# Kernel tuning notes

Hardware: AMD Instinct MI355X
Metric: run time of the kernel (lower is better)

Reference implementation:

```python
import jax, jax.numpy as jnp
import numpy as np

EMB = 128
HEADS = 4
OUT = EMB // HEADS
NL = 50000
NR = 50000
E = 800000


def setup_inputs() -> dict:
    key = jax.random.key(0)
    ks = jax.random.split(key, 20)
    s = 0.05  # param init scale
    f32 = jnp.float32
    return {
        "left_features": jax.random.normal(ks[0], (NL, EMB), f32),
        "edge_indices": jax.random.randint(ks[1], (2, E), 0, NL),  # NL == NR
        "edge_features": jax.random.normal(ks[2], (E, EMB), f32),
        "right_features": jax.random.normal(ks[3], (NR, EMB), f32),
        # GATv2Conv params
        "W_l": jax.random.normal(ks[4], (EMB, HEADS * OUT), f32) * s,
        "b_l": jnp.zeros((HEADS * OUT,), f32),
        "W_r": jax.random.normal(ks[5], (EMB, HEADS * OUT), f32) * s,
        "b_r": jnp.zeros((HEADS * OUT,), f32),
        "W_e": jax.random.normal(ks[6], (EMB, HEADS * OUT), f32) * s,
        "att": jax.random.normal(ks[7], (HEADS, OUT), f32) * s,
        "b_conv": jnp.zeros((HEADS * OUT,), f32),
        # LayerNorm
        "ln_g": jnp.ones((EMB,), f32),
        "ln_b": jnp.zeros((EMB,), f32),
        # output MLP
        "W1": jax.random.normal(ks[8], (2 * EMB, EMB), f32) * s,
        "b1": jnp.zeros((EMB,), f32),
        "W2": jax.random.normal(ks[9], (EMB, EMB), f32) * s,
        "b2": jnp.zeros((EMB,), f32),
    }


def reference(left_features, edge_indices, edge_features, right_features,
              W_l, b_l, W_r, b_r, W_e, att, b_conv, ln_g, ln_b,
              W1, b1, W2, b2):
    H, O = att.shape
    n_right = right_features.shape[0]
    src = edge_indices[0]
    dst = edge_indices[1]

    # linear projections (GATv2: separate lin_l for src, lin_r for dst, lin_edge no bias)
    x_l = (left_features @ W_l + b_l).reshape(-1, H, O)   # [NL,H,O]
    x_r = (right_features @ W_r + b_r).reshape(-1, H, O)  # [NR,H,O]
    e = (edge_features @ W_e).reshape(-1, H, O)           # [E,H,O]

    # per-edge GATv2 attention logits
    z = jax.nn.leaky_relu(x_l[src] + x_r[dst] + e, 0.2)   # [E,H,O]
    logits = jnp.einsum('eho,ho->eh', z, att)             # [E,H]

    # segment softmax over destination nodes
    m = jax.ops.segment_max(logits, dst, num_segments=n_right)
    m = jnp.where(jnp.isfinite(m), m, 0.0)  # guard empty segments
    ex = jnp.exp(logits - m[dst])
    den = jax.ops.segment_sum(ex, dst, num_segments=n_right)
    alpha = ex / (den[dst] + 1e-16)                       # [E,H]

    # message = transformed src feature weighted by alpha, scatter-add to dst
    msg = jax.ops.segment_sum(x_l[src] * alpha[:, :, None], dst,
                              num_segments=n_right)       # [NR,H,O]
    msg = msg.reshape(n_right, H * O) + b_conv            # concat heads + bias

    # LayerNorm
    mu = jnp.mean(msg, axis=-1, keepdims=True)
    var = jnp.mean(jnp.square(msg - mu), axis=-1, keepdims=True)
    msg = (msg - mu) * jax.lax.rsqrt(var + 1e-5) * ln_g + ln_b

    # out MLP on [msg, right_features]
    h = jnp.concatenate([msg, right_features], axis=-1)
    h = jax.nn.relu(h @ W1 + b1)
    return h @ W2 + b2
```

## Files before the change

### kernel.cpp

```cpp
#include <hip/hip_runtime.h>
#include <math.h>

#define EMB 128

typedef __bf16 bf16x8 __attribute__((ext_vector_type(8)));
typedef float f32x4 __attribute__((ext_vector_type(4)));


__device__ __forceinline__ int incl_scan_256(int v, int* lds) {
    int tid = threadIdx.x;
    lds[tid] = v;
    __syncthreads();
    #pragma unroll
    for (int off = 1; off < 256; off <<= 1) {
        int t = (tid >= off) ? lds[tid - off] : 0;
        __syncthreads();
        lds[tid] += t;
        __syncthreads();
    }
    return lds[tid];
}

__global__ void pack_all_kernel(
    const float* __restrict__ W_e, const float* __restrict__ W_l,
    const float* __restrict__ W_r, const float* __restrict__ W1,
    const float* __restrict__ W2,
    __bf16* __restrict__ we, __bf16* __restrict__ wl, __bf16* __restrict__ wr,
    __bf16* __restrict__ w1, __bf16* __restrict__ w2)
{
    int idx = blockIdx.x * 256 + threadIdx.x;
    const float* W; __bf16* P; int K; int base;
    if (idx < 2048)       { W = W_e; P = we; K = 128; base = 0; }
    else if (idx < 4096)  { W = W_l; P = wl; K = 128; base = 2048; }
    else if (idx < 6144)  { W = W_r; P = wr; K = 128; base = 4096; }
    else if (idx < 10240) { W = W1;  P = w1; K = 256; base = 6144; }
    else                  { W = W2;  P = w2; K = 128; base = 10240; }
    idx -= base;
    const int ksteps = K >> 5;
    const int l = idx & 63;
    const int s = (idx >> 6) % ksteps;
    const int t = (idx >> 6) / ksteps;
    #pragma unroll
    for (int j = 0; j < 8; ++j) {
        int k = s * 32 + ((l >> 4) * 8) + j;
        int n = t * 16 + (l & 15);
        P[(size_t)idx * 8 + j] = (__bf16)W[(size_t)k * EMB + n];
    }
}

__device__ __forceinline__ void proj4_compute(
    const __bf16* Wl, const float* __restrict__ X, const float* __restrict__ bias,
    float* __restrict__ Y, int M, int relu, int blk, int tid)
{
    const int l = tid & 63, wv = tid >> 6;
    const int q = l >> 4, c = l & 15;
    const int rbase = blk * 64 + wv * 16;

    int arow = rbase + c; if (arow >= M) arow = M - 1;
    const float* Ap = X + (size_t)arow * EMB + q * 8;

    f32x4 acc[8];
    #pragma unroll
    for (int t = 0; t < 8; ++t) acc[t] = (f32x4){0.f, 0.f, 0.f, 0.f};

    #pragma unroll
    for (int s = 0; s < 4; ++s) {
        float4 a0 = *(const float4*)(Ap + s * 32);
        float4 a1 = *(const float4*)(Ap + s * 32 + 4);
        bf16x8 af;
        af[0] = (__bf16)a0.x; af[1] = (__bf16)a0.y; af[2] = (__bf16)a0.z; af[3] = (__bf16)a0.w;
        af[4] = (__bf16)a1.x; af[5] = (__bf16)a1.y; af[6] = (__bf16)a1.z; af[7] = (__bf16)a1.w;
        #pragma unroll
        for (int t = 0; t < 8; ++t) {
            bf16x8 bf = *reinterpret_cast<const bf16x8*>(&Wl[((size_t)(t * 4 + s) * 64 + l) * 8]);
            acc[t] = __builtin_amdgcn_mfma_f32_16x16x32_bf16(af, bf, acc[t], 0, 0, 0);
        }
    }

    const int r0 = rbase + q * 4;
    #pragma unroll
    for (int t = 0; t < 8; ++t) {
        const int col = t * 16 + c;
        const float b = bias ? bias[col] : 0.f;
        #pragma unroll
        for (int i = 0; i < 4; ++i) {
            const int r = r0 + i;
            if (r < M) {
                float v = acc[t][i] + b;
                if (relu) v = fmaxf(v, 0.f);
                Y[(size_t)r * EMB + col] = v;
            }
        }
    }
}

template<int KSTEPS>
__global__ __launch_bounds__(256) void proj_mfma(
    const float* __restrict__ X0, const float* __restrict__ X1,
    const __bf16* __restrict__ wpack, const float* __restrict__ bias,
    float* __restrict__ Y, int M, int relu)
{
    __shared__ __attribute__((aligned(16))) __bf16 Wl[KSTEPS * 8 * 64 * 8];
    const int tid = threadIdx.x;
    #pragma unroll
    for (int i = tid; i < KSTEPS * 512; i += 256)
        ((float4*)Wl)[i] = ((const float4*)wpack)[i];
    __syncthreads();

    const int l = tid & 63, wv = tid >> 6;
    const int q = l >> 4, c = l & 15;
    const int rbase = blockIdx.x * 64 + wv * 16;

    int arow = rbase + c; if (arow >= M) arow = M - 1;
    const float* Ap0 = X0 + (size_t)arow * EMB + q * 8;
    const float* Ap1 = (KSTEPS == 8) ? (X1 + (size_t)arow * EMB + q * 8) : Ap0;

    f32x4 acc[8];
    #pragma unroll
    for (int t = 0; t < 8; ++t) acc[t] = (f32x4){0.f, 0.f, 0.f, 0.f};

    #pragma unroll
    for (int s = 0; s < KSTEPS; ++s) {
        const float* bp = (s < 4) ? Ap0 : Ap1;
        const int ss = (s < 4) ? s : s - 4;
        float4 a0 = *(const float4*)(bp + ss * 32);
        float4 a1 = *(const float4*)(bp + ss * 32 + 4);
        bf16x8 af;
        af[0] = (__bf16)a0.x; af[1] = (__bf16)a0.y; af[2] = (__bf16)a0.z; af[3] = (__bf16)a0.w;
        af[4] = (__bf16)a1.x; af[5] = (__bf16)a1.y; af[6] = (__bf16)a1.z; af[7] = (__bf16)a1.w;
        #pragma unroll
        for (int t = 0; t < 8; ++t) {
            bf16x8 bf = *reinterpret_cast<const bf16x8*>(&Wl[((size_t)(t * KSTEPS + s) * 64 + l) * 8]);
            acc[t] = __builtin_amdgcn_mfma_f32_16x16x32_bf16(af, bf, acc[t], 0, 0, 0);
        }
    }

    const int r0 = rbase + q * 4;
    #pragma unroll
    for (int t = 0; t < 8; ++t) {
        const int col = t * 16 + c;
        const float b = bias ? bias[col] : 0.f;
        #pragma unroll
        for (int i = 0; i < 4; ++i) {
            const int r = r0 + i;
            if (r < M) {
                float v = acc[t][i] + b;
                if (relu) v = fmaxf(v, 0.f);
                Y[(size_t)r * EMB + col] = v;
            }
        }
    }
}

__global__ __launch_bounds__(256) void proj_dual(
    const float* __restrict__ XA, const __bf16* __restrict__ wpA,
    const float* __restrict__ bA, float* __restrict__ YA, int MA, int gA,
    const float* __restrict__ XB, const __bf16* __restrict__ wpB,
    const float* __restrict__ bB, float* __restrict__ YB, int MB)
{
    __shared__ __attribute__((aligned(16))) __bf16 Wl[4 * 8 * 64 * 8];
    const int tid = threadIdx.x;
    const bool second = (blockIdx.x >= gA);
    const __bf16* wp = second ? wpB : wpA;
    #pragma unroll
    for (int i = tid; i < 2048; i += 256)
        ((float4*)Wl)[i] = ((const float4*)wp)[i];
    __syncthreads();
    if (second) proj4_compute(Wl, XB, bB, YB, MB, 0, blockIdx.x - gA, tid);
    else        proj4_compute(Wl, XA, bA, YA, MA, 0, blockIdx.x, tid);
}

__global__ __launch_bounds__(256) void edge_kernel(
    const float* __restrict__ EF, const __bf16* __restrict__ wpack,
    const float* __restrict__ xl, const float* __restrict__ xr,
    const int* __restrict__ src, const int* __restrict__ dst,
    const int* __restrict__ pos,
    const float* __restrict__ att, float* __restrict__ exb, int En)
{
    __shared__ __attribute__((aligned(16))) __bf16 Wl[EMB * EMB];
    const int tid = threadIdx.x;
    {
        float4* d4 = (float4*)Wl;
        const float4* s4 = (const float4*)wpack;
        #pragma unroll
        for (int i = 0; i < 8; ++i) d4[tid + 256 * i] = s4[tid + 256 * i];
    }

    const int l = tid & 63, wv = tid >> 6;
    const int q = l >> 4, c = l & 15;
    const int ebase = blockIdx.x * 64 + wv * 16;
    const int e0 = ebase + q * 4;

    int ses[4], des[4];
    #pragma unroll
    for (int i = 0; i < 4; ++i) {
        int ei = e0 + i; if (ei >= En) ei = En - 1;
        ses[i] = src[ei]; des[i] = dst[ei];
    }
    float attv[8];
    #pragma unroll
    for (int t = 0; t < 8; ++t) attv[t] = att[t * 16 + c];

    __syncthreads();

    f32x4 acc[8];
    #pragma unroll
    for (int t = 0; t < 8; ++t) acc[t] = (f32x4){0.f, 0.f, 0.f, 0.f};

    int arow = ebase + c; if (arow >= En) arow = En - 1;
    const float* Ap = EF + (size_t)arow * EMB + q * 8;

    #pragma unroll
    for (int s = 0; s < 4; ++s) {
        float4 a0 = *(const float4*)(Ap + s * 32);
        float4 a1 = *(const float4*)(Ap + s * 32 + 4);
        bf16x8 af;
        af[0] = (__bf16)a0.x; af[1] = (__bf16)a0.y; af[2] = (__bf16)a0.z; af[3] = (__bf16)a0.w;
        af[4] = (__bf16)a1.x; af[5] = (__bf16)a1.y; af[6] = (__bf16)a1.z; af[7] = (__bf16)a1.w;
        #pragma unroll
        for (int t = 0; t < 8; ++t) {
            bf16x8 bf = *reinterpret_cast<const bf16x8*>(&Wl[((size_t)(t * 4 + s) * 64 + l) * 8]);
            acc[t] = __builtin_amdgcn_mfma_f32_16x16x32_bf16(af, bf, acc[t], 0, 0, 0);
        }
    }

    float v[4][4];
    #pragma unroll
    for (int i = 0; i < 4; ++i) {
        const float* xls = xl + (size_t)ses[i] * EMB;
        const float* xrs = xr + (size_t)des[i] * EMB;
        float ph[4] = {0.f, 0.f, 0.f, 0.f};
        #pragma unroll
        for (int t = 0; t < 8; ++t) {
            int col = t * 16 + c;
            float z = acc[t][i] + xls[col] + xrs[col];
            z = (z > 0.f) ? z : 0.2f * z;
            ph[t >> 1] += z * attv[t];
        }
        #pragma unroll
        for (int h = 0; h < 4; ++h) v[i][h] = ph[h];
    }

    #pragma unroll
    for (int m = 1; m < 16; m <<= 1) {
        #pragma unroll
        for (int i = 0; i < 4; ++i)
            #pragma unroll
            for (int h = 0; h < 4; ++h)
                v[i][h] += __shfl_xor(v[i][h], m);
    }

    const int si = c >> 2, sh = c & 3;
    float val = v[0][0];
    #pragma unroll
    for (int i = 0; i < 4; ++i)
        #pragma unroll
        for (int h = 0; h < 4; ++h)
            if (si == i && sh == h) val = v[i][h];
    const int ew = e0 + si;
    if (ew < En) {
        int p = pos[ew];
        exb[(size_t)p * 4 + sh] = expf(val);
    }
}

__global__ void hist_kernel(const int* __restrict__ dst, int* __restrict__ counts, int En) {
    int i = blockIdx.x * 256 + threadIdx.x;
    if (i < En) atomicAdd(&counts[dst[i]], 1);
}

__global__ void scan1_kernel(const int* __restrict__ counts, int* __restrict__ bsum, int N) {
    __shared__ int red[4];
    int i = blockIdx.x * 256 + threadIdx.x;
    int v = (i < N) ? counts[i] : 0;
    #pragma unroll
    for (int m = 1; m < 64; m <<= 1) v += __shfl_xor(v, m);
    if ((threadIdx.x & 63) == 0) red[threadIdx.x >> 6] = v;
    __syncthreads();
    if (threadIdx.x == 0) bsum[blockIdx.x] = red[0] + red[1] + red[2] + red[3];
}

__global__ void scan2_kernel(int* __restrict__ bsum, int* __restrict__ boff, int nb,
                             int* __restrict__ offs, int NRtot, int Etot) {
    __shared__ int lds[256];
    int tid = threadIdx.x;
    int v = (tid < nb) ? bsum[tid] : 0;
    int incl = incl_scan_256(v, lds);
    if (tid < nb) boff[tid] = incl - v;
    if (tid == 0) offs[NRtot] = Etot;
}

__global__ void scan3_kernel(const int* __restrict__ counts, const int* __restrict__ boff,
                             int* __restrict__ offs, int* __restrict__ cursor, int N) {
    __shared__ int lds[256];
    int tid = threadIdx.x;
    int i = blockIdx.x * 256 + tid;
    int v = (i < N) ? counts[i] : 0;
    int incl = incl_scan_256(v, lds);
    int excl = incl - v + boff[blockIdx.x];
    if (i < N) { offs[i] = excl; cursor[i] = excl; }
}

__global__ void scatter_kernel(const int* __restrict__ dst, const int* __restrict__ srcv,
                               int* __restrict__ cursor, int* __restrict__ pos,
                               int* __restrict__ src_sorted, int En) {
    int i = blockIdx.x * 256 + threadIdx.x;
    if (i < En) {
        int p = atomicAdd(&cursor[dst[i]], 1);
        pos[i] = p;
        src_sorted[p] = srcv[i];
    }
}

__global__ __launch_bounds__(128) void msg_ln_kernel(
    const float* __restrict__ xl, const float* __restrict__ exb,
    const int* __restrict__ src_sorted, const int* __restrict__ offs,
    const float* __restrict__ bconv,
    const float* __restrict__ ln_g, const float* __restrict__ ln_b,
    float* __restrict__ msg)
{
    const int d = blockIdx.x;
    const int tid = threadIdx.x;
    const int h = tid >> 5;
    const int beg = offs[d], end = offs[d + 1];
    const float bc = bconv[tid], g = ln_g[tid], bb = ln_b[tid];

    float acc = 0.f, den = 0.f;
    int i = beg;
    for (; i + 4 <= end; i += 4) {
        int s0 = src_sorted[i + 0], s1 = src_sorted[i + 1];
        int s2 = src_sorted[i + 2], s3 = src_sorted[i + 3];
        float ev0 = exb[(size_t)(i + 0) * 4 + h];
        float ev1 = exb[(size_t)(i + 1) * 4 + h];
        float ev2 = exb[(size_t)(i + 2) * 4 + h];
        float ev3 = exb[(size_t)(i + 3) * 4 + h];
        float x0 = xl[(size_t)s0 * EMB + tid];
        float x1 = xl[(size_t)s1 * EMB + tid];
        float x2 = xl[(size_t)s2 * EMB + tid];
        float x3 = xl[(size_t)s3 * EMB + tid];
        acc += ev0 * x0; den += ev0;
        acc += ev1 * x1; den += ev1;
        acc += ev2 * x2; den += ev2;
        acc += ev3 * x3; den += ev3;
    }
    for (; i < end; ++i) {
        int s = src_sorted[i];
        float ev = exb[(size_t)i * 4 + h];
        acc += ev * xl[(size_t)s * EMB + tid];
        den += ev;
    }
    float m = acc / (den + 1e-16f) + bc;

    __shared__ float red[2];
    float s1 = m;
    #pragma unroll
    for (int mk = 1; mk < 64; mk <<= 1) s1 += __shfl_xor(s1, mk);
    if ((tid & 63) == 0) red[tid >> 6] = s1;
    __syncthreads();
    float mu = (red[0] + red[1]) * (1.f / EMB);
    __syncthreads();
    float cm = m - mu;
    float s2 = cm * cm;
    #pragma unroll
    for (int mk = 1; mk < 64; mk <<= 1) s2 += __shfl_xor(s2, mk);
    if ((tid & 63) == 0) red[tid >> 6] = s2;
    __syncthreads();
    float var = (red[0] + red[1]) * (1.f / EMB);
    float y = cm * (1.f / sqrtf(var + 1e-5f)) * g + bb;
    msg[(size_t)d * EMB + tid] = y;
}

extern "C" void kernel_launch(void* const* d_in, const int* in_sizes, int n_in,
                              void* d_out, int out_size, void* d_ws, size_t ws_size,
                              hipStream_t stream) {
    const float* left  = (const float*)d_in[0];
    const int*   eidx  = (const int*)d_in[1];
    const float* ef    = (const float*)d_in[2];
    const float* right = (const float*)d_in[3];
    const float* W_l   = (const float*)d_in[4];
    const float* b_l   = (const float*)d_in[5];
    const float* W_r   = (const float*)d_in[6];
    const float* b_r   = (const float*)d_in[7];
    const float* W_e   = (const float*)d_in[8];
    const float* att   = (const float*)d_in[9];
    const float* bconv = (const float*)d_in[10];
    const float* ln_g  = (const float*)d_in[11];
    const float* ln_b  = (const float*)d_in[12];
    const float* W1    = (const float*)d_in[13];
    const float* b1    = (const float*)d_in[14];
    const float* W2    = (const float*)d_in[15];
    const float* b2    = (const float*)d_in[16];

    const int NLn = in_sizes[0] / EMB;
    const int En  = in_sizes[1] / 2;
    const int NRn = in_sizes[3] / EMB;
    const int* src  = eidx;
    const int* dstp = eidx + En;

    __bf16* we_pack = (__bf16*)d_ws;
    __bf16* wl_pack = we_pack + 16384;
    __bf16* wr_pack = wl_pack + 16384;
    __bf16* w1_pack = wr_pack + 16384;
    __bf16* w2_pack = w1_pack + 32768;
    float* fws = (float*)d_ws + 49152;
    size_t off = 0;
    float* x_l = fws + off; off += (size_t)NLn * EMB;
    float* x_r = fws + off; off += (size_t)NRn * EMB;
    float* exb = fws + off; off += (size_t)En * 4;
    float* msg = fws + off; off += (size_t)NRn * EMB;
    int* counts     = (int*)(fws + off);
    int* offs       = counts + NRn;
    int* cursor     = offs + NRn + 1;
    int* bsum       = cursor + NRn;
    int* boff       = bsum + 256;
    int* pos        = boff + 256;
    int* src_sorted = pos + En;

    const int nb = (NRn + 255) / 256;
    const int gP_L = (NLn + 63) / 64;
    const int gP_R = (NRn + 63) / 64;
    const int gE64 = (En + 63) / 64;
    const int gE256 = (En + 255) / 256;

    hipMemsetAsync(counts, 0, (size_t)NRn * sizeof(int), stream);

    pack_all_kernel<<<48, 256, 0, stream>>>(W_e, W_l, W_r, W1, W2,
                                            we_pack, wl_pack, wr_pack, w1_pack, w2_pack);

    proj_dual<<<gP_L + gP_R, 256, 0, stream>>>(left, wl_pack, b_l, x_l, NLn, gP_L,
                                               right, wr_pack, b_r, x_r, NRn);

    hist_kernel<<<gE256, 256, 0, stream>>>(dstp, counts, En);
    scan1_kernel<<<nb, 256, 0, stream>>>(counts, bsum, NRn);
    scan2_kernel<<<1, 256, 0, stream>>>(bsum, boff, nb, offs, NRn, En);
    scan3_kernel<<<nb, 256, 0, stream>>>(counts, boff, offs, cursor, NRn);
    scatter_kernel<<<gE256, 256, 0, stream>>>(dstp, src, cursor, pos, src_sorted, En);

    edge_kernel<<<gE64, 256, 0, stream>>>(ef, we_pack, x_l, x_r, src, dstp, pos, att, exb, En);

    msg_ln_kernel<<<NRn, 128, 0, stream>>>(x_l, exb, src_sorted, offs, bconv, ln_g, ln_b, msg);

    proj_mfma<8><<<gP_R, 256, 0, stream>>>(msg, right, w1_pack, b1, x_r, NRn, 1);
    proj_mfma<4><<<gP_R, 256, 0, stream>>>(x_r, nullptr, w2_pack, b2, (float*)d_out, NRn, 0);
}
```

Before: 901.4 us.

## Process edges in dst-sorted order and restage attention epilogue through LDS

The scatter step now writes one packed int4 record per sorted slot (original edge id, src, dst). The edge kernel walks edges in dst-sorted order, gathering edge-feature rows by original id, and writes exp-logits contiguously by slot instead of scattering through a pos array. The epilogue stages MFMA results into swizzled LDS so each lane handles one edge-head pair with vectorized float4 loads of x_l, x_r and att, replacing the 16-lane shuffle reduction. In exchange, edge-feature reads become random gathers of full rows, and the edge kernel needs an extra barrier and LDS reuse.

After: 953.4 us. 5.8% more time.

```diff
diff --git a/kernel.cpp b/kernel.cpp
--- a/kernel.cpp
+++ b/kernel.cpp
@@ -173,9 +173,8 @@
 __global__ __launch_bounds__(256) void edge_kernel(
     const float* __restrict__ EF, const __bf16* __restrict__ wpack,
     const float* __restrict__ xl, const float* __restrict__ xr,
-    const int* __restrict__ src, const int* __restrict__ dst,
-    const int* __restrict__ pos,
-    const float* __restrict__ att, float* __restrict__ exb, int En)
+    const int4* __restrict__ edat, const float* __restrict__ att,
+    float* __restrict__ exb, int En)
 {
     __shared__ __attribute__((aligned(16))) __bf16 Wl[EMB * EMB];
     const int tid = threadIdx.x;
@@ -188,27 +187,17 @@
 
     const int l = tid & 63, wv = tid >> 6;
     const int q = l >> 4, c = l & 15;
-    const int ebase = blockIdx.x * 64 + wv * 16;
-    const int e0 = ebase + q * 4;
-
-    int ses[4], des[4];
-    #pragma unroll
-    for (int i = 0; i < 4; ++i) {
-        int ei = e0 + i; if (ei >= En) ei = En - 1;
-        ses[i] = src[ei]; des[i] = dst[ei];
-    }
-    float attv[8];
-    #pragma unroll
-    for (int t = 0; t < 8; ++t) attv[t] = att[t * 16 + c];
+    const int sbase = blockIdx.x * 64 + wv * 16;
+
+    int aslot = sbase + c; if (aslot >= En) aslot = En - 1;
+    const int efrow = edat[aslot].x;
+    const float* Ap = EF + (size_t)efrow * EMB + q * 8;
 
     __syncthreads();
 
     f32x4 acc[8];
     #pragma unroll
     for (int t = 0; t < 8; ++t) acc[t] = (f32x4){0.f, 0.f, 0.f, 0.f};
-
-    int arow = ebase + c; if (arow >= En) arow = En - 1;
-    const float* Ap = EF + (size_t)arow * EMB + q * 8;
 
     #pragma unroll
     for (int s = 0; s < 4; ++s) {
@@ -224,44 +213,40 @@
         }
     }
 
-    float v[4][4];
-    #pragma unroll
-    for (int i = 0; i < 4; ++i) {
-        const float* xls = xl + (size_t)ses[i] * EMB;
-        const float* xrs = xr + (size_t)des[i] * EMB;
-        float ph[4] = {0.f, 0.f, 0.f, 0.f};
-        #pragma unroll
-        for (int t = 0; t < 8; ++t) {
-            int col = t * 16 + c;
-            float z = acc[t][i] + xls[col] + xrs[col];
-            z = (z > 0.f) ? z : 0.2f * z;
-            ph[t >> 1] += z * attv[t];
-        }
-        #pragma unroll
-        for (int h = 0; h < 4; ++h) v[i][h] = ph[h];
-    }
-
-    #pragma unroll
-    for (int m = 1; m < 16; m <<= 1) {
-        #pragma unroll
-        for (int i = 0; i < 4; ++i)
-            #pragma unroll
-            for (int h = 0; h < 4; ++h)
-                v[i][h] += __shfl_xor(v[i][h], m);
-    }
-
-    const int si = c >> 2, sh = c & 3;
-    float val = v[0][0];
-    #pragma unroll
-    for (int i = 0; i < 4; ++i)
-        #pragma unroll
-        for (int h = 0; h < 4; ++h)
-            if (si == i && sh == h) val = v[i][h];
-    const int ew = e0 + si;
-    if (ew < En) {
-        int p = pos[ew];
-        exb[(size_t)p * 4 + sh] = expf(val);
-    }
+    __syncthreads();
+
+    float* Z = (float*)Wl + wv * 2048;
+    #pragma unroll
+    for (int t = 0; t < 8; ++t) {
+        const int col = t * 16 + c;
+        #pragma unroll
+        for (int i = 0; i < 4; ++i) {
+            const int le = q * 4 + i;
+            Z[le * 128 + (col ^ ((le & 7) << 2))] = acc[t][i];
+        }
+    }
+
+    const int e = l >> 2, h = l & 3;
+    const int slot = sbase + e;
+    const int slotc = (slot < En) ? slot : En - 1;
+    const int4 ed = edat[slotc];
+    const float* xls = xl + (size_t)ed.y * EMB + h * 32;
+    const float* xrs = xr + (size_t)ed.z * EMB + h * 32;
+    const float* atp = att + h * 32;
+
+    float p = 0.f;
+    #pragma unroll
+    for (int j4 = 0; j4 < 8; ++j4) {
+        f32x4 z4 = *(const f32x4*)&Z[e * 128 + ((h * 32 + j4 * 4) ^ ((e & 7) << 2))];
+        float4 a4 = *(const float4*)(xls + j4 * 4);
+        float4 b4 = *(const float4*)(xrs + j4 * 4);
+        float4 t4 = *(const float4*)(atp + j4 * 4);
+        float z0 = z4[0] + a4.x + b4.x; z0 = (z0 > 0.f) ? z0 : 0.2f * z0; p += z0 * t4.x;
+        float z1 = z4[1] + a4.y + b4.y; z1 = (z1 > 0.f) ? z1 : 0.2f * z1; p += z1 * t4.y;
+        float z2 = z4[2] + a4.z + b4.z; z2 = (z2 > 0.f) ? z2 : 0.2f * z2; p += z2 * t4.z;
+        float z3 = z4[3] + a4.w + b4.w; z3 = (z3 > 0.f) ? z3 : 0.2f * z3; p += z3 * t4.w;
+    }
+    if (slot < En) exb[(size_t)slot * 4 + h] = expf(p);
 }
 
 __global__ void hist_kernel(const int* __restrict__ dst, int* __restrict__ counts, int En) {
@@ -302,19 +287,18 @@
 }
 
 __global__ void scatter_kernel(const int* __restrict__ dst, const int* __restrict__ srcv,
-                               int* __restrict__ cursor, int* __restrict__ pos,
-                               int* __restrict__ src_sorted, int En) {
+                               int* __restrict__ cursor, int4* __restrict__ edat, int En) {
     int i = blockIdx.x * 256 + threadIdx.x;
     if (i < En) {
-        int p = atomicAdd(&cursor[dst[i]], 1);
-        pos[i] = p;
-        src_sorted[p] = srcv[i];
+        int d = dst[i];
+        int p = atomicAdd(&cursor[d], 1);
+        edat[p] = make_int4(i, srcv[i], d, 0);
     }
 }
 
 __global__ __launch_bounds__(128) void msg_ln_kernel(
     const float* __restrict__ xl, const float* __restrict__ exb,
-    const int* __restrict__ src_sorted, const int* __restrict__ offs,
+    const int4* __restrict__ edat, const int* __restrict__ offs,
     const float* __restrict__ bconv,
     const float* __restrict__ ln_g, const float* __restrict__ ln_b,
     float* __restrict__ msg)
@@ -328,8 +312,8 @@
     float acc = 0.f, den = 0.f;
     int i = beg;
     for (; i + 4 <= end; i += 4) {
-        int s0 = src_sorted[i + 0], s1 = src_sorted[i + 1];
-        int s2 = src_sorted[i + 2], s3 = src_sorted[i + 3];
+        int s0 = edat[i + 0].y, s1 = edat[i + 1].y;
+        int s2 = edat[i + 2].y, s3 = edat[i + 3].y;
         float ev0 = exb[(size_t)(i + 0) * 4 + h];
         float ev1 = exb[(size_t)(i + 1) * 4 + h];
         float ev2 = exb[(size_t)(i + 2) * 4 + h];
@@ -344,7 +328,7 @@
         acc += ev3 * x3; den += ev3;
     }
     for (; i < end; ++i) {
-        int s = src_sorted[i];
+        int s = edat[i].y;
         float ev = exb[(size_t)i * 4 + h];
         acc += ev * xl[(size_t)s * EMB + tid];
         den += ev;
@@ -352,18 +336,18 @@
     float m = acc / (den + 1e-16f) + bc;
 
     __shared__ float red[2];
-    float s1 = m;
-    #pragma unroll
-    for (int mk = 1; mk < 64; mk <<= 1) s1 += __shfl_xor(s1, mk);
-    if ((tid & 63) == 0) red[tid >> 6] = s1;
+    float s1v = m;
+    #pragma unroll
+    for (int mk = 1; mk < 64; mk <<= 1) s1v += __shfl_xor(s1v, mk);
+    if ((tid & 63) == 0) red[tid >> 6] = s1v;
     __syncthreads();
     float mu = (red[0] + red[1]) * (1.f / EMB);
     __syncthreads();
     float cm = m - mu;
-    float s2 = cm * cm;
-    #pragma unroll
-    for (int mk = 1; mk < 64; mk <<= 1) s2 += __shfl_xor(s2, mk);
-    if ((tid & 63) == 0) red[tid >> 6] = s2;
+    float s2v = cm * cm;
+    #pragma unroll
+    for (int mk = 1; mk < 64; mk <<= 1) s2v += __shfl_xor(s2v, mk);
+    if ((tid & 63) == 0) red[tid >> 6] = s2v;
     __syncthreads();
     float var = (red[0] + red[1]) * (1.f / EMB);
     float y = cm * (1.f / sqrtf(var + 1e-5f)) * g + bb;
@@ -408,13 +392,12 @@
     float* x_r = fws + off; off += (size_t)NRn * EMB;
     float* exb = fws + off; off += (size_t)En * 4;
     float* msg = fws + off; off += (size_t)NRn * EMB;
-    int* counts     = (int*)(fws + off);
-    int* offs       = counts + NRn;
-    int* cursor     = offs + NRn + 1;
-    int* bsum       = cursor + NRn;
-    int* boff       = bsum + 256;
-    int* pos        = boff + 256;
-    int* src_sorted = pos + En;
+    int4* edat  = (int4*)(fws + off);
+    int* counts = (int*)(edat + En);
+    int* offs   = counts + NRn;
+    int* cursor = offs + NRn + 1;
+    int* bsum   = cursor + NRn;
+    int* boff   = bsum + 256;
 
     const int nb = (NRn + 255) / 256;
     const int gP_L = (NLn + 63) / 64;
@@ -434,11 +417,11 @@
     scan1_kernel<<<nb, 256, 0, stream>>>(counts, bsum, NRn);
     scan2_kernel<<<1, 256, 0, stream>>>(bsum, boff, nb, offs, NRn, En);
     scan3_kernel<<<nb, 256, 0, stream>>>(counts, boff, offs, cursor, NRn);
-    scatter_kernel<<<gE256, 256, 0, stream>>>(dstp, src, cursor, pos, src_sorted, En);
-
-    edge_kernel<<<gE64, 256, 0, stream>>>(ef, we_pack, x_l, x_r, src, dstp, pos, att, exb, En);
-
-    msg_ln_kernel<<<NRn, 128, 0, stream>>>(x_l, exb, src_sorted, offs, bconv, ln_g, ln_b, msg);
+    scatter_kernel<<<gE256, 256, 0, stream>>>(dstp, src, cursor, edat, En);
+
+    edge_kernel<<<gE64, 256, 0, stream>>>(ef, we_pack, x_l, x_r, edat, att, exb, En);
+
+    msg_ln_kernel<<<NRn, 128, 0, stream>>>(x_l, exb, edat, offs, bconv, ln_g, ln_b, msg);
 
     proj_mfma<8><<<gP_R, 256, 0, stream>>>(msg, right, w1_pack, b1, x_r, NRn, 1);
     proj_mfma<4><<<gP_R, 256, 0, stream>>>(x_r, nullptr, w2_pack, b2, (float*)d_out, NRn, 0);
```

## Make edge kernel persistent over tiles with early gathers; deepen msg loop unroll

Applied to the files above, without the earlier changes.

The edge kernel now runs a fixed grid of about 1792 blocks, each looping over several 64-edge tiles. This spreads the 32KB per-block weight copy into LDS over more edges. Inside each tile, the edge-feature rows, the x_l gathers and the pos lookup are issued before the MFMAs so their latency overlaps the math, and launch bounds ask for 3 blocks per CU. The message aggregation loop is unrolled from 4 to 8 edges so more independent gathers are in flight. The cost is higher register pressure from the prefetched arrays, which could reduce occupancy or cause spills.

Result: slower. 1.101 ms (+22.2%).

```diff
diff --git a/kernel.cpp b/kernel.cpp
--- a/kernel.cpp
+++ b/kernel.cpp
@@ -170,12 +170,12 @@
     else        proj4_compute(Wl, XA, bA, YA, MA, 0, blockIdx.x, tid);
 }
 
-__global__ __launch_bounds__(256) void edge_kernel(
+__global__ __launch_bounds__(256, 3) void edge_kernel(
     const float* __restrict__ EF, const __bf16* __restrict__ wpack,
     const float* __restrict__ xl, const float* __restrict__ xr,
     const int* __restrict__ src, const int* __restrict__ dst,
-    const int* __restrict__ pos,
-    const float* __restrict__ att, float* __restrict__ exb, int En)
+    const int* __restrict__ pos, const float* __restrict__ att,
+    float* __restrict__ exb, int En, int tpb, int nt)
 {
     __shared__ __attribute__((aligned(16))) __bf16 Wl[EMB * EMB];
     const int tid = threadIdx.x;
@@ -188,79 +188,104 @@
 
     const int l = tid & 63, wv = tid >> 6;
     const int q = l >> 4, c = l & 15;
-    const int ebase = blockIdx.x * 64 + wv * 16;
-    const int e0 = ebase + q * 4;
-
-    int ses[4], des[4];
-    #pragma unroll
-    for (int i = 0; i < 4; ++i) {
-        int ei = e0 + i; if (ei >= En) ei = En - 1;
-        ses[i] = src[ei]; des[i] = dst[ei];
-    }
+    const int si = c >> 2, sh = c & 3;
+
     float attv[8];
     #pragma unroll
     for (int t = 0; t < 8; ++t) attv[t] = att[t * 16 + c];
 
     __syncthreads();
 
-    f32x4 acc[8];
-    #pragma unroll
-    for (int t = 0; t < 8; ++t) acc[t] = (f32x4){0.f, 0.f, 0.f, 0.f};
-
-    int arow = ebase + c; if (arow >= En) arow = En - 1;
-    const float* Ap = EF + (size_t)arow * EMB + q * 8;
-
-    #pragma unroll
-    for (int s = 0; s < 4; ++s) {
-        float4 a0 = *(const float4*)(Ap + s * 32);
-        float4 a1 = *(const float4*)(Ap + s * 32 + 4);
-        bf16x8 af;
-        af[0] = (__bf16)a0.x; af[1] = (__bf16)a0.y; af[2] = (__bf16)a0.z; af[3] = (__bf16)a0.w;
-        af[4] = (__bf16)a1.x; af[5] = (__bf16)a1.y; af[6] = (__bf16)a1.z; af[7] = (__bf16)a1.w;
-        #pragma unroll
-        for (int t = 0; t < 8; ++t) {
-            bf16x8 bf = *reinterpret_cast<const bf16x8*>(&Wl[((size_t)(t * 4 + s) * 64 + l) * 8]);
-            acc[t] = __builtin_amdgcn_mfma_f32_16x16x32_bf16(af, bf, acc[t], 0, 0, 0);
-        }
-    }
-
-    float v[4][4];
-    #pragma unroll
-    for (int i = 0; i < 4; ++i) {
-        const float* xls = xl + (size_t)ses[i] * EMB;
-        const float* xrs = xr + (size_t)des[i] * EMB;
-        float ph[4] = {0.f, 0.f, 0.f, 0.f};
-        #pragma unroll
-        for (int t = 0; t < 8; ++t) {
-            int col = t * 16 + c;
-            float z = acc[t][i] + xls[col] + xrs[col];
-            z = (z > 0.f) ? z : 0.2f * z;
-            ph[t >> 1] += z * attv[t];
-        }
-        #pragma unroll
-        for (int h = 0; h < 4; ++h) v[i][h] = ph[h];
-    }
-
-    #pragma unroll
-    for (int m = 1; m < 16; m <<= 1) {
+    const int t0 = blockIdx.x * tpb;
+    const int t1 = (t0 + tpb < nt) ? (t0 + tpb) : nt;
+
+    for (int tile = t0; tile < t1; ++tile) {
+        const int ebase = tile * 64 + wv * 16;
+
+        int arow = ebase + c; if (arow >= En) arow = En - 1;
+        const float* Ap = EF + (size_t)arow * EMB + q * 8;
+        float4 a0p[4], a1p[4];
+        #pragma unroll
+        for (int s = 0; s < 4; ++s) {
+            a0p[s] = *(const float4*)(Ap + s * 32);
+            a1p[s] = *(const float4*)(Ap + s * 32 + 4);
+        }
+
+        int se[4], de[4];
+        #pragma unroll
+        for (int i = 0; i < 4; ++i) {
+            int er = ebase + q * 4 + i; if (er >= En) er = En - 1;
+            se[i] = src[er]; de[i] = dst[er];
+        }
+        int ewr = ebase + q * 4 + si;
+        const int ewc = (ewr < En) ? ewr : En - 1;
+        const int pe = pos[ewc];
+
+        float xlv[4][8];
+        #pragma unroll
+        for (int i = 0; i < 4; ++i) {
+            const float* xp = xl + (size_t)se[i] * EMB + c;
+            #pragma unroll
+            for (int t = 0; t < 8; ++t) xlv[i][t] = xp[t * 16];
+        }
+
+        f32x4 acc[8];
+        #pragma unroll
+        for (int t = 0; t < 8; ++t) acc[t] = (f32x4){0.f, 0.f, 0.f, 0.f};
+
+        #pragma unroll
+        for (int s = 0; s < 4; ++s) {
+            bf16x8 af;
+            af[0] = (__bf16)a0p[s].x; af[1] = (__bf16)a0p[s].y;
+            af[2] = (__bf16)a0p[s].z; af[3] = (__bf16)a0p[s].w;
+            af[4] = (__bf16)a1p[s].x; af[5] = (__bf16)a1p[s].y;
+            af[6] = (__bf16)a1p[s].z; af[7] = (__bf16)a1p[s].w;
+            #pragma unroll
+            for (int t = 0; t < 8; ++t) {
+                bf16x8 bf = *reinterpret_cast<const bf16x8*>(&Wl[((size_t)(t * 4 + s) * 64 + l) * 8]);
+                acc[t] = __builtin_amdgcn_mfma_f32_16x16x32_bf16(af, bf, acc[t], 0, 0, 0);
+            }
+        }
+
+        float xrv[4][8];
+        #pragma unroll
+        for (int i = 0; i < 4; ++i) {
+            const float* xp = xr + (size_t)de[i] * EMB + c;
+            #pragma unroll
+            for (int t = 0; t < 8; ++t) xrv[i][t] = xp[t * 16];
+        }
+
+        float vv[4][4];
+        #pragma unroll
+        for (int i = 0; i < 4; ++i) {
+            float ph[4] = {0.f, 0.f, 0.f, 0.f};
+            #pragma unroll
+            for (int t = 0; t < 8; ++t) {
+                float z = acc[t][i] + xlv[i][t] + xrv[i][t];
+                z = (z > 0.f) ? z : 0.2f * z;
+                ph[t >> 1] += z * attv[t];
+            }
+            #pragma unroll
+            for (int h = 0; h < 4; ++h) vv[i][h] = ph[h];
+        }
+
+        #pragma unroll
+        for (int m = 1; m < 16; m <<= 1) {
+            #pragma unroll
+            for (int i = 0; i < 4; ++i)
+                #pragma unroll
+                for (int h = 0; h < 4; ++h)
+                    vv[i][h] += __shfl_xor(vv[i][h], m);
+        }
+
+        float val = vv[0][0];
         #pragma unroll
         for (int i = 0; i < 4; ++i)
             #pragma unroll
             for (int h = 0; h < 4; ++h)
-                v[i][h] += __shfl_xor(v[i][h], m);
-    }
-
-    const int si = c >> 2, sh = c & 3;
-    float val = v[0][0];
-    #pragma unroll
-    for (int i = 0; i < 4; ++i)
-        #pragma unroll
-        for (int h = 0; h < 4; ++h)
-            if (si == i && sh == h) val = v[i][h];
-    const int ew = e0 + si;
-    if (ew < En) {
-        int p = pos[ew];
-        exb[(size_t)p * 4 + sh] = expf(val);
+                if (si == i && sh == h) val = vv[i][h];
+
+        if (ewr < En) exb[(size_t)pe * 4 + sh] = expf(val);
     }
 }
 
@@ -327,21 +352,17 @@
 
     float acc = 0.f, den = 0.f;
     int i = beg;
-    for (; i + 4 <= end; i += 4) {
-        int s0 = src_sorted[i + 0], s1 = src_sorted[i + 1];
-        int s2 = src_sorted[i + 2], s3 = src_sorted[i + 3];
-        float ev0 = exb[(size_t)(i + 0) * 4 + h];
-        float ev1 = exb[(size_t)(i + 1) * 4 + h];
-        float ev2 = exb[(size_t)(i + 2) * 4 + h];
-        float ev3 = exb[(size_t)(i + 3) * 4 + h];
-        float x0 = xl[(size_t)s0 * EMB + tid];
-        float x1 = xl[(size_t)s1 * EMB + tid];
-        float x2 = xl[(size_t)s2 * EMB + tid];
-        float x3 = xl[(size_t)s3 * EMB + tid];
-        acc += ev0 * x0; den += ev0;
-        acc += ev1 * x1; den += ev1;
-        acc += ev2 * x2; den += ev2;
-        acc += ev3 * x3; den += ev3;
+    for (; i + 8 <= end; i += 8) {
+        int sv[8]; float ev[8];
+        #pragma unroll
+        for (int k = 0; k < 8; ++k) sv[k] = src_sorted[i + k];
+        #pragma unroll
+        for (int k = 0; k < 8; ++k) ev[k] = exb[(size_t)(i + k) * 4 + h];
+        float xv[8];
+        #pragma unroll
+        for (int k = 0; k < 8; ++k) xv[k] = xl[(size_t)sv[k] * EMB + tid];
+        #pragma unroll
+        for (int k = 0; k < 8; ++k) { acc += ev[k] * xv[k]; den += ev[k]; }
     }
     for (; i < end; ++i) {
         int s = src_sorted[i];
@@ -352,18 +373,18 @@
     float m = acc / (den + 1e-16f) + bc;
 
     __shared__ float red[2];
-    float s1 = m;
-    #pragma unroll
-    for (int mk = 1; mk < 64; mk <<= 1) s1 += __shfl_xor(s1, mk);
-    if ((tid & 63) == 0) red[tid >> 6] = s1;
+    float s1v = m;
+    #pragma unroll
+    for (int mk = 1; mk < 64; mk <<= 1) s1v += __shfl_xor(s1v, mk);
+    if ((tid & 63) == 0) red[tid >> 6] = s1v;
     __syncthreads();
     float mu = (red[0] + red[1]) * (1.f / EMB);
     __syncthreads();
     float cm = m - mu;
-    float s2 = cm * cm;
-    #pragma unroll
-    for (int mk = 1; mk < 64; mk <<= 1) s2 += __shfl_xor(s2, mk);
-    if ((tid & 63) == 0) red[tid >> 6] = s2;
+    float s2v = cm * cm;
+    #pragma unroll
+    for (int mk = 1; mk < 64; mk <<= 1) s2v += __shfl_xor(s2v, mk);
+    if ((tid & 63) == 0) red[tid >> 6] = s2v;
     __syncthreads();
     float var = (red[0] + red[1]) * (1.f / EMB);
     float y = cm * (1.f / sqrtf(var + 1e-5f)) * g + bb;
@@ -419,8 +440,12 @@
     const int nb = (NRn + 255) / 256;
     const int gP_L = (NLn + 63) / 64;
     const int gP_R = (NRn + 63) / 64;
-    const int gE64 = (En + 63) / 64;
     const int gE256 = (En + 255) / 256;
+
+    const int nt = (En + 63) / 64;
+    const int nblocks = 1792;
+    const int tpb = (nt + nblocks - 1) / nblocks;
+    const int active = (nt + tpb - 1) / tpb;
 
     hipMemsetAsync(counts, 0, (size_t)NRn * sizeof(int), stream);
 
@@ -436,7 +461,8 @@
     scan3_kernel<<<nb, 256, 0, stream>>>(counts, boff, offs, cursor, NRn);
     scatter_kernel<<<gE256, 256, 0, stream>>>(dstp, src, cursor, pos, src_sorted, En);
 
-    edge_kernel<<<gE64, 256, 0, stream>>>(ef, we_pack, x_l, x_r, src, dstp, pos, att, exb, En);
+    edge_kernel<<<active, 256, 0, stream>>>(ef, we_pack, x_l, x_r, src, dstp, pos,
+                                            att, exb, En, tpb, nt);
 
     msg_ln_kernel<<<NRn, 128, 0, stream>>>(x_l, exb, src_sorted, offs, bconv, ln_g, ln_b, msg);
 
```
